# Optimization experiments

Measured on AMD Instinct MI355X. Metric: run time of the kernel, lower is better.

## Reference

```python
import jax, jax.numpy as jnp
import numpy as np

IN_CH, OUT_CH, K, DIL, COND = 16, 16, 3, 4, 8
B, T_OUT = 32, 65536
PAD = DIL * (K - 1)


def setup_inputs() -> dict:
    key = jax.random.key(0)
    ks = jax.random.split(key, 6)
    return {
        "x": jax.random.normal(ks[0], (B, IN_CH, T_OUT + PAD), dtype=jnp.float32),
        "p": jax.random.normal(ks[1], (B, COND), dtype=jnp.float32),
        "W1": jax.random.normal(ks[2], (COND, IN_CH), dtype=jnp.float32) * 0.3,
        "b1": jax.random.normal(ks[3], (IN_CH,), dtype=jnp.float32) * 0.1,
        "W2": jax.random.normal(ks[4], (IN_CH, IN_CH * OUT_CH * K), dtype=jnp.float32) * 0.1,
        "b2": jax.random.normal(ks[5], (IN_CH * OUT_CH * K,), dtype=jnp.float32) * 0.05,
    }


def reference(x, p, W1, b1, W2, b2):
    # hypernetwork: per-sample conv weights from condition vector p
    h = p @ W1 + b1                      # [B, in_ch]
    h = jnp.where(h > 0, h, 0.2 * h)     # LeakyReLU(0.2)
    w = (h @ W2 + b2).reshape(B, IN_CH * K, OUT_CH)  # [B, in_ch*K, out_ch]

    # im2col-style gather of K dilated shifted slices, concatenated on channel dim
    start, end = PAD, x.shape[-1]
    x_cat = jnp.concatenate(
        [x[:, :, start - i * DIL : end - i * DIL] for i in range(K)], axis=1
    )  # [B, in_ch*K, T_out]

    # batched GEMM: [B, T, in_ch*K] x [B, in_ch*K, out_ch] -> output [B, out_ch, T]
    y = jnp.einsum("bct,bco->bot", x_cat, w)
    return y
```

## Files before the change

kernel.cpp:

```cpp
#include <hip/hip_runtime.h>


#define NB 32
#define IN_CH 16
#define OUT_CH 16
#define KW 3
#define DIL 4
#define COND 8
#define T_OUT 65536
#define PADT 8
#define XT (T_OUT + PADT)
#define W2COLS (IN_CH * OUT_CH * KW)
#define TPB 256
#define TPT 4
#define T_PER_BLOCK (TPB * TPT)
#define BLOCKS_PER_B (T_OUT / T_PER_BLOCK)

__global__ __launch_bounds__(TPB)
void hyperconv_kernel(const float* __restrict__ x,
                      const float* __restrict__ p,
                      const float* __restrict__ W1,
                      const float* __restrict__ b1,
                      const float* __restrict__ W2,
                      const float* __restrict__ b2,
                      float* __restrict__ y)
{
    __shared__ float h_lds[IN_CH];
    __shared__ float w_lds[W2COLS];

    const int tid    = threadIdx.x;
    const int b      = blockIdx.x / BLOCKS_PER_B;
    const int tchunk = blockIdx.x % BLOCKS_PER_B;

    if (tid < IN_CH) {
        float acc = b1[tid];
#pragma unroll
        for (int j = 0; j < COND; ++j)
            acc += p[b * COND + j] * W1[j * IN_CH + tid];
        h_lds[tid] = acc > 0.f ? acc : 0.2f * acc;
    }
    __syncthreads();

#pragma unroll
    for (int r = 0; r < 3; ++r) {
        const int n = tid * 3 + r;
        float acc = b2[n];
#pragma unroll
        for (int c = 0; c < IN_CH; ++c)
            acc += h_lds[c] * W2[c * W2COLS + n];
        w_lds[n] = acc;
    }
    __syncthreads();

    const int t0 = tchunk * T_PER_BLOCK + tid * TPT;
    const float* xb = x + (size_t)b * IN_CH * XT + t0;

    float4 acc[OUT_CH];
#pragma unroll
    for (int o = 0; o < OUT_CH; ++o) acc[o] = make_float4(0.f, 0.f, 0.f, 0.f);

#pragma unroll
    for (int c = 0; c < IN_CH; ++c) {
        const float4 a0 = *(const float4*)(xb + c * XT);
        const float4 a1 = *(const float4*)(xb + c * XT + 4);
        const float4 a2 = *(const float4*)(xb + c * XT + 8);
        const float4 vs[KW] = {a2, a1, a0};
#pragma unroll
        for (int i = 0; i < KW; ++i) {
            const float4 v = vs[i];
            const float* wrow = &w_lds[(i * IN_CH + c) * OUT_CH];
#pragma unroll
            for (int og = 0; og < 4; ++og) {
                const float4 wv = *(const float4*)(wrow + og * 4);
                float4* a = &acc[og * 4];
                a[0].x += v.x * wv.x; a[0].y += v.y * wv.x;
                a[0].z += v.z * wv.x; a[0].w += v.w * wv.x;
                a[1].x += v.x * wv.y; a[1].y += v.y * wv.y;
                a[1].z += v.z * wv.y; a[1].w += v.w * wv.y;
                a[2].x += v.x * wv.z; a[2].y += v.y * wv.z;
                a[2].z += v.z * wv.z; a[2].w += v.w * wv.z;
                a[3].x += v.x * wv.w; a[3].y += v.y * wv.w;
                a[3].z += v.z * wv.w; a[3].w += v.w * wv.w;
            }
        }
    }

    float* yb = y + (size_t)b * OUT_CH * T_OUT + t0;
#pragma unroll
    for (int o = 0; o < OUT_CH; ++o)
        *(float4*)(yb + o * T_OUT) = acc[o];
}

extern "C" void kernel_launch(void* const* d_in, const int* in_sizes, int n_in,
                              void* d_out, int out_size, void* d_ws, size_t ws_size,
                              hipStream_t stream) {
    const float* x  = (const float*)d_in[0];
    const float* p  = (const float*)d_in[1];
    const float* W1 = (const float*)d_in[2];
    const float* b1 = (const float*)d_in[3];
    const float* W2 = (const float*)d_in[4];
    const float* b2 = (const float*)d_in[5];
    float* y = (float*)d_out;

    dim3 grid(NB * BLOCKS_PER_B);
    dim3 block(TPB);
    hyperconv_kernel<<<grid, block, 0, stream>>>(x, p, W1, b1, W2, b2, y);
}
```

Before: 248.4 us.

## Stage x rows into LDS with async global_load_lds multi-buffer pipeline

Replaces the direct per-thread global loads of x (which read overlapping windows three times per thread) with a 4-deep ring of LDS row buffers filled via global_load_lds. Loads for upcoming input channels are issued ahead while the current channel is computed, synchronized with manual vmcnt waits and barriers. Output stores become nontemporal. This adds LDS usage, per-channel barriers, and fragile hand-tuned waitcnt counts in exchange for overlapping memory with compute.

```diff
diff --git a/kernel.cpp b/kernel.cpp
--- a/kernel.cpp
+++ b/kernel.cpp
@@ -15,6 +15,50 @@
 #define TPT 4
 #define T_PER_BLOCK (TPB * TPT)
 #define BLOCKS_PER_B (T_OUT / T_PER_BLOCK)
+#define ROWF (T_PER_BLOCK + PADT)
+#define NBUF 4
+
+typedef const __attribute__((address_space(1))) void* gvp;
+typedef __attribute__((address_space(3))) void* svp;
+typedef float f32x4 __attribute__((ext_vector_type(4)));
+
+__device__ __forceinline__ void stage_row(const float* __restrict__ g,
+                                          float* l, int wid, int lane)
+{
+    __builtin_amdgcn_global_load_lds((gvp)(g + wid * 256 + lane * 4),
+                                     (svp)(l + wid * 256), 16, 0, 0);
+    if (wid == 0 && lane < 2)
+        __builtin_amdgcn_global_load_lds((gvp)(g + 1024 + lane * 4),
+                                         (svp)(l + 1024), 16, 0, 0);
+}
+
+__device__ __forceinline__ void compute_row(const float* __restrict__ xrow,
+                                            const float* __restrict__ w_lds,
+                                            int c, float4* acc, int tid)
+{
+    const float4 l0 = *(const float4*)(xrow + tid * 4);
+    const float4 l1 = *(const float4*)(xrow + tid * 4 + 4);
+    const float4 l2 = *(const float4*)(xrow + tid * 4 + 8);
+    const float4 vs[KW] = {l2, l1, l0};
+#pragma unroll
+    for (int i = 0; i < KW; ++i) {
+        const float4 v = vs[i];
+        const float* wrow = w_lds + (i * IN_CH + c) * OUT_CH;
+#pragma unroll
+        for (int og = 0; og < 4; ++og) {
+            const float4 wv = *(const float4*)(wrow + og * 4);
+            float4* a = acc + og * 4;
+            a[0].x += v.x * wv.x; a[0].y += v.y * wv.x;
+            a[0].z += v.z * wv.x; a[0].w += v.w * wv.x;
+            a[1].x += v.x * wv.y; a[1].y += v.y * wv.y;
+            a[1].z += v.z * wv.y; a[1].w += v.w * wv.y;
+            a[2].x += v.x * wv.z; a[2].y += v.y * wv.z;
+            a[2].z += v.z * wv.z; a[2].w += v.w * wv.z;
+            a[3].x += v.x * wv.w; a[3].y += v.y * wv.w;
+            a[3].z += v.z * wv.w; a[3].w += v.w * wv.w;
+        }
+    }
+}
 
 __global__ __launch_bounds__(TPB)
 void hyperconv_kernel(const float* __restrict__ x,
@@ -25,12 +69,22 @@
                       const float* __restrict__ b2,
                       float* __restrict__ y)
 {
+    __shared__ __align__(16) float xbuf[NBUF][ROWF];
     __shared__ float h_lds[IN_CH];
-    __shared__ float w_lds[W2COLS];
+    __shared__ __align__(16) float w_lds[W2COLS];
 
     const int tid    = threadIdx.x;
+    const int wid    = tid >> 6;
+    const int lane   = tid & 63;
     const int b      = blockIdx.x / BLOCKS_PER_B;
     const int tchunk = blockIdx.x % BLOCKS_PER_B;
+    const int t0b    = tchunk * T_PER_BLOCK;
+
+    const float* xrb = x + (size_t)b * IN_CH * XT + t0b;
+
+    stage_row(xrb + 0 * XT, xbuf[0], wid, lane);
+    stage_row(xrb + 1 * XT, xbuf[1], wid, lane);
+    stage_row(xrb + 2 * XT, xbuf[2], wid, lane);
 
     if (tid < IN_CH) {
         float acc = b1[tid];
@@ -52,43 +106,35 @@
     }
     __syncthreads();
 
-    const int t0 = tchunk * T_PER_BLOCK + tid * TPT;
-    const float* xb = x + (size_t)b * IN_CH * XT + t0;
-
     float4 acc[OUT_CH];
 #pragma unroll
     for (int o = 0; o < OUT_CH; ++o) acc[o] = make_float4(0.f, 0.f, 0.f, 0.f);
 
+    for (int c = 0; c < 13; ++c) {
+        __builtin_amdgcn_sched_barrier(0);
+        stage_row(xrb + (c + 3) * XT, xbuf[(c + 3) & 3], wid, lane);
+        if (wid == 0) asm volatile("s_waitcnt vmcnt(6)" ::: "memory");
+        else          asm volatile("s_waitcnt vmcnt(3)" ::: "memory");
+        __builtin_amdgcn_s_barrier();
+        __builtin_amdgcn_sched_barrier(0);
+        compute_row(xbuf[c & 3], w_lds, c, acc, tid);
+        __builtin_amdgcn_sched_barrier(0);
+        __builtin_amdgcn_s_barrier();
+    }
+    asm volatile("s_waitcnt vmcnt(0)" ::: "memory");
+    __builtin_amdgcn_s_barrier();
+    __builtin_amdgcn_sched_barrier(0);
+    compute_row(xbuf[13 & 3], w_lds, 13, acc, tid);
+    compute_row(xbuf[14 & 3], w_lds, 14, acc, tid);
+    compute_row(xbuf[15 & 3], w_lds, 15, acc, tid);
+
+    float* yb = y + (size_t)b * OUT_CH * T_OUT + t0b + tid * TPT;
 #pragma unroll
-    for (int c = 0; c < IN_CH; ++c) {
-        const float4 a0 = *(const float4*)(xb + c * XT);
-        const float4 a1 = *(const float4*)(xb + c * XT + 4);
-        const float4 a2 = *(const float4*)(xb + c * XT + 8);
-        const float4 vs[KW] = {a2, a1, a0};
-#pragma unroll
-        for (int i = 0; i < KW; ++i) {
-            const float4 v = vs[i];
-            const float* wrow = &w_lds[(i * IN_CH + c) * OUT_CH];
-#pragma unroll
-            for (int og = 0; og < 4; ++og) {
-                const float4 wv = *(const float4*)(wrow + og * 4);
-                float4* a = &acc[og * 4];
-                a[0].x += v.x * wv.x; a[0].y += v.y * wv.x;
-                a[0].z += v.z * wv.x; a[0].w += v.w * wv.x;
-                a[1].x += v.x * wv.y; a[1].y += v.y * wv.y;
-                a[1].z += v.z * wv.y; a[1].w += v.w * wv.y;
-                a[2].x += v.x * wv.z; a[2].y += v.y * wv.z;
-                a[2].z += v.z * wv.z; a[2].w += v.w * wv.z;
-                a[3].x += v.x * wv.w; a[3].y += v.y * wv.w;
-                a[3].z += v.z * wv.w; a[3].w += v.w * wv.w;
-            }
-        }
+    for (int o = 0; o < OUT_CH; ++o) {
+        const float4 a = acc[o];
+        f32x4 v = {a.x, a.y, a.z, a.w};
+        __builtin_nontemporal_store(v, (f32x4*)(yb + o * T_OUT));
     }
-
-    float* yb = y + (size_t)b * OUT_CH * T_OUT + t0;
-#pragma unroll
-    for (int o = 0; o < OUT_CH; ++o)
-        *(float4*)(yb + o * T_OUT) = acc[o];
 }
 
 extern "C" void kernel_launch(void* const* d_in, const int* in_sizes, int n_in,
```

Result: no change. 246.1 us (-0.9%).

## Stage x rows into LDS via async global_load_lds with per-row waitcnt pipelining

Applied to the files above, without the earlier changes.

Each wave copies its 16 input-channel rows (256 samples plus 8 halo) straight from global memory into LDS with global_load_lds. It then starts computing on each row as soon as that row's load finishes, using descending vmcnt waits. This replaces the three overlapping float4 global loads per thread per channel with one staged copy, and overlaps load latency with FMA work. Output stores become nontemporal. The hand-written vmcnt counts depend on the exact number of loads issued per lane (lanes 0-1 issue two), which is fragile, and the unaligned LDS reads at lane*4+4/+8 may cause bank conflicts.

```diff
diff --git a/kernel.cpp b/kernel.cpp
--- a/kernel.cpp
+++ b/kernel.cpp
@@ -5,7 +5,6 @@
 #define IN_CH 16
 #define OUT_CH 16
 #define KW 3
-#define DIL 4
 #define COND 8
 #define T_OUT 65536
 #define PADT 8
@@ -14,7 +13,50 @@
 #define TPB 256
 #define TPT 4
 #define T_PER_BLOCK (TPB * TPT)
+#define T_PER_WAVE 256
 #define BLOCKS_PER_B (T_OUT / T_PER_BLOCK)
+#define WROW (T_PER_WAVE + PADT)
+
+typedef const __attribute__((address_space(1))) void* gvp;
+typedef __attribute__((address_space(3))) void* svp;
+typedef float f32x4 __attribute__((ext_vector_type(4)));
+
+__device__ __forceinline__ void stage_wrow(const float* __restrict__ g,
+                                           float* l, int lane)
+{
+    __builtin_amdgcn_global_load_lds((gvp)(g + lane * 4), (svp)l, 16, 0, 0);
+    if (lane < 2)
+        __builtin_amdgcn_global_load_lds((gvp)(g + T_PER_WAVE + lane * 4),
+                                         (svp)(l + T_PER_WAVE), 16, 0, 0);
+}
+
+__device__ __forceinline__ void compute_row(const float* __restrict__ xrow,
+                                            const float* __restrict__ w_lds,
+                                            int c, float4* acc, int lane)
+{
+    const float4 l0 = *(const float4*)(xrow + lane * 4);
+    const float4 l1 = *(const float4*)(xrow + lane * 4 + 4);
+    const float4 l2 = *(const float4*)(xrow + lane * 4 + 8);
+    const float4 vs[KW] = {l2, l1, l0};
+#pragma unroll
+    for (int i = 0; i < KW; ++i) {
+        const float4 v = vs[i];
+        const float* wrow = w_lds + (i * IN_CH + c) * OUT_CH;
+#pragma unroll
+        for (int og = 0; og < 4; ++og) {
+            const float4 wv = *(const float4*)(wrow + og * 4);
+            float4* a = acc + og * 4;
+            a[0].x += v.x * wv.x; a[0].y += v.y * wv.x;
+            a[0].z += v.z * wv.x; a[0].w += v.w * wv.x;
+            a[1].x += v.x * wv.y; a[1].y += v.y * wv.y;
+            a[1].z += v.z * wv.y; a[1].w += v.w * wv.y;
+            a[2].x += v.x * wv.z; a[2].y += v.y * wv.z;
+            a[2].z += v.z * wv.z; a[2].w += v.w * wv.z;
+            a[3].x += v.x * wv.w; a[3].y += v.y * wv.w;
+            a[3].z += v.z * wv.w; a[3].w += v.w * wv.w;
+        }
+    }
+}
 
 __global__ __launch_bounds__(TPB)
 void hyperconv_kernel(const float* __restrict__ x,
@@ -25,12 +67,16 @@
                       const float* __restrict__ b2,
                       float* __restrict__ y)
 {
+    __shared__ __align__(16) float xr[4][IN_CH][WROW];
     __shared__ float h_lds[IN_CH];
-    __shared__ float w_lds[W2COLS];
+    __shared__ __align__(16) float w_lds[W2COLS];
 
     const int tid    = threadIdx.x;
+    const int wid    = tid >> 6;
+    const int lane   = tid & 63;
     const int b      = blockIdx.x / BLOCKS_PER_B;
     const int tchunk = blockIdx.x % BLOCKS_PER_B;
+    const int t0b    = tchunk * T_PER_BLOCK;
 
     if (tid < IN_CH) {
         float acc = b1[tid];
@@ -52,43 +98,32 @@
     }
     __syncthreads();
 
-    const int t0 = tchunk * T_PER_BLOCK + tid * TPT;
-    const float* xb = x + (size_t)b * IN_CH * XT + t0;
+    const float* xwb = x + (size_t)b * IN_CH * XT + t0b + wid * T_PER_WAVE;
+#pragma unroll
+    for (int c = 0; c < IN_CH; ++c)
+        stage_wrow(xwb + c * XT, &xr[wid][c][0], lane);
+    __builtin_amdgcn_sched_barrier(0);
 
     float4 acc[OUT_CH];
 #pragma unroll
     for (int o = 0; o < OUT_CH; ++o) acc[o] = make_float4(0.f, 0.f, 0.f, 0.f);
 
+#define STEP(R, V) \
+    asm volatile("s_waitcnt vmcnt(" #V ")" ::: "memory"); \
+    compute_row(&xr[wid][R][0], w_lds, R, acc, lane);
+    STEP(0, 30)  STEP(1, 28)  STEP(2, 26)  STEP(3, 24)
+    STEP(4, 22)  STEP(5, 20)  STEP(6, 18)  STEP(7, 16)
+    STEP(8, 14)  STEP(9, 12)  STEP(10, 10) STEP(11, 8)
+    STEP(12, 6)  STEP(13, 4)  STEP(14, 2)  STEP(15, 0)
+#undef STEP
+
+    float* yb = y + (size_t)b * OUT_CH * T_OUT + t0b + wid * T_PER_WAVE + lane * TPT;
 #pragma unroll
-    for (int c = 0; c < IN_CH; ++c) {
-        const float4 a0 = *(const float4*)(xb + c * XT);
-        const float4 a1 = *(const float4*)(xb + c * XT + 4);
-        const float4 a2 = *(const float4*)(xb + c * XT + 8);
-        const float4 vs[KW] = {a2, a1, a0};
-#pragma unroll
-        for (int i = 0; i < KW; ++i) {
-            const float4 v = vs[i];
-            const float* wrow = &w_lds[(i * IN_CH + c) * OUT_CH];
-#pragma unroll
-            for (int og = 0; og < 4; ++og) {
-                const float4 wv = *(const float4*)(wrow + og * 4);
-                float4* a = &acc[og * 4];
-                a[0].x += v.x * wv.x; a[0].y += v.y * wv.x;
-                a[0].z += v.z * wv.x; a[0].w += v.w * wv.x;
-                a[1].x += v.x * wv.y; a[1].y += v.y * wv.y;
-                a[1].z += v.z * wv.y; a[1].w += v.w * wv.y;
-                a[2].x += v.x * wv.z; a[2].y += v.y * wv.z;
-                a[2].z += v.z * wv.z; a[2].w += v.w * wv.z;
-                a[3].x += v.x * wv.w; a[3].y += v.y * wv.w;
-                a[3].z += v.z * wv.w; a[3].w += v.w * wv.w;
-            }
-        }
+    for (int o = 0; o < OUT_CH; ++o) {
+        const float4 a = acc[o];
+        f32x4 v = {a.x, a.y, a.z, a.w};
+        __builtin_nontemporal_store(v, (f32x4*)(yb + o * T_OUT));
     }
-
-    float* yb = y + (size_t)b * OUT_CH * T_OUT + t0;
-#pragma unroll
-    for (int o = 0; o < OUT_CH; ++o)
-        *(float4*)(yb + o * T_OUT) = acc[o];
 }
 
 extern "C" void kernel_launch(void* const* d_in, const int* in_sizes, int n_in,
```

Result: faster. 243.2 us (-2.1%).
